# Performance work log

Hardware: AMD Instinct MI355X
Metric: run time of the kernel (lower is better)

## Reference

```python
import jax, jax.numpy as jnp
import numpy as np

N, E, IN_DIM, HID, OUT = 50000, 800000, 256, 128, 128
EPS_BN = 1e-5
EPS_NORM = 1e-12


def leaky(x):
    return jnp.where(x >= 0, x, 0.2 * x)


def batchnorm(x, gamma, beta):
    # training-mode BatchNorm1d over node dimension
    mean = jnp.mean(x, axis=0)
    var = jnp.var(x, axis=0)
    return gamma * (x - mean) * jax.lax.rsqrt(var + EPS_BN) + beta


def sage_conv(x, src, dst, W_l, b_l, W_r):
    # PyG SAGEConv (mean aggr): lin_l(mean_{j->i} x_j) + lin_r(x_i)
    msg = x[src]  # [E, D] gather
    agg = jax.ops.segment_sum(msg, dst, num_segments=N)
    cnt = jax.ops.segment_sum(jnp.ones((E,), x.dtype), dst, num_segments=N)
    agg = agg / jnp.maximum(cnt, 1.0)[:, None]
    return agg @ W_l + b_l + x @ W_r


def setup_inputs() -> dict:
    key = jax.random.key(0)
    ks = jax.random.split(key, 16)
    s = lambda fan_in: (2.0 / fan_in) ** 0.5
    return {
        "x": jax.random.normal(ks[0], (N, IN_DIM), jnp.float32),
        "edge_index": jax.random.randint(ks[1], (2, E), 0, N),
        "W_in": jax.random.normal(ks[2], (IN_DIM, HID), jnp.float32) * s(IN_DIM),
        "b_in": jnp.zeros((HID,), jnp.float32),
        "g1": jnp.ones((HID,), jnp.float32),
        "be1": jnp.zeros((HID,), jnp.float32),
        "Wl1": jax.random.normal(ks[3], (HID, HID), jnp.float32) * s(HID),
        "bl1": jnp.zeros((HID,), jnp.float32),
        "Wr1": jax.random.normal(ks[4], (HID, HID), jnp.float32) * s(HID),
        "Wl2": jax.random.normal(ks[5], (HID, OUT), jnp.float32) * s(HID),
        "bl2": jnp.zeros((OUT,), jnp.float32),
        "Wr2": jax.random.normal(ks[6], (HID, OUT), jnp.float32) * s(HID),
        "Wskip": jax.random.normal(ks[7], (HID, OUT), jnp.float32) * s(HID),
        "bskip": jnp.zeros((OUT,), jnp.float32),
        "g2": jnp.ones((OUT,), jnp.float32),
        "be2": jnp.zeros((OUT,), jnp.float32),
    }


def reference(x, edge_index, W_in, b_in, g1, be1, Wl1, bl1, Wr1, Wl2, bl2, Wr2, Wskip, bskip, g2, be2):
    src, dst = edge_index[0], edge_index[1]
    h = batchnorm(leaky(x @ W_in + b_in), g1, be1)
    skip = h
    h1 = leaky(sage_conv(h, src, dst, Wl1, bl1, Wr1))  # dropout = identity (eval)
    h2 = sage_conv(h1, src, dst, Wl2, bl2, Wr2)
    out = h2 + (skip @ Wskip + bskip)
    out = batchnorm(out, g2, be2)
    norm = jnp.sqrt(jnp.sum(out * out, axis=1, keepdims=True))
    return out / jnp.maximum(norm, EPS_NORM)
```

## Files before the change

kernel.cpp:

```cpp
#include <hip/hip_runtime.h>
#include <math.h>

#define N_NODES 50000
#define N_EDGES 800000
#define IN_DIM 256
#define HID 128
#define ZPITCH 384

typedef unsigned short u16;
typedef u16 u16x8 __attribute__((ext_vector_type(8)));
typedef u16 u16x2 __attribute__((ext_vector_type(2)));
typedef __bf16 bf16x8 __attribute__((ext_vector_type(8)));
typedef float f32x4 __attribute__((ext_vector_type(4)));

#define AS1 __attribute__((address_space(1)))
#define AS3 __attribute__((address_space(3)))

union F8 { u16x8 u; bf16x8 h; };

__device__ __forceinline__ u16 f2b(float f) {
    unsigned u = __builtin_bit_cast(unsigned, f);
    u = (u + 0x7FFFu + ((u >> 16) & 1u)) >> 16;
    return (u16)u;
}
__device__ __forceinline__ float b2f(u16 h) {
    unsigned u = ((unsigned)h) << 16;
    return __builtin_bit_cast(float, u);
}

template<int A_F32> struct ARaw;
template<> struct ARaw<0> { u16x8 v; };
template<> struct ARaw<1> { float4 f0, f1; };

template<int A_F32>
__device__ __forceinline__ ARaw<A_F32> load_raw(const void* base, size_t row, int P, int koff);
template<>
__device__ __forceinline__ ARaw<0> load_raw<0>(const void* base, size_t row, int P, int koff) {
    ARaw<0> r;
    r.v = *reinterpret_cast<const u16x8*>((const u16*)base + row * P + koff);
    return r;
}
template<>
__device__ __forceinline__ ARaw<1> load_raw<1>(const void* base, size_t row, int P, int koff) {
    ARaw<1> r;
    const float* p = (const float*)base + row * P + koff;
    r.f0 = *reinterpret_cast<const float4*>(p);
    r.f1 = *reinterpret_cast<const float4*>(p + 4);
    return r;
}

template<int A_F32>
__device__ __forceinline__ F8 to_frag(const ARaw<A_F32>& r);
template<>
__device__ __forceinline__ F8 to_frag<0>(const ARaw<0>& r) { F8 f; f.u = r.v; return f; }
template<>
__device__ __forceinline__ F8 to_frag<1>(const ARaw<1>& r) {
    F8 f;
    f.h[0] = (__bf16)r.f0.x; f.h[1] = (__bf16)r.f0.y;
    f.h[2] = (__bf16)r.f0.z; f.h[3] = (__bf16)r.f0.w;
    f.h[4] = (__bf16)r.f1.x; f.h[5] = (__bf16)r.f1.y;
    f.h[6] = (__bf16)r.f1.z; f.h[7] = (__bf16)r.f1.w;
    return f;
}

template<int LEAKY, int STATS, int OUT_BF16, int A_F32, int NC>
__global__ __launch_bounds__(512, 2) void gemm_mfma(
    int M, const void* __restrict__ A, int P,
    const u16* __restrict__ Wf,
    const float* __restrict__ bias0,
    void* __restrict__ Cout, int CP,
    float* __restrict__ stats)
{
    __shared__ u16 Bs[NC * 4096];

    const int t   = threadIdx.x;
    const int w   = t >> 6;
    const int l   = t & 63;
    const int l15 = l & 15;
    const int lg  = l >> 4;
    const int rb  = blockIdx.x * 256 + w * 32;

    int r0 = rb + l15;
    int r1 = r0 + 16;
    size_t r0c = (size_t)(r0 < M ? r0 : M - 1);
    size_t r1c = (size_t)(r1 < M ? r1 : M - 1);
    const int ko = lg * 8;

#pragma unroll
    for (int i = 0; i < NC; ++i) {
        int idx = i * 512 + t;
        __builtin_amdgcn_global_load_lds(
            (const AS1 void*)(Wf + (size_t)idx * 8),
            (AS3 void*)(Bs + (size_t)idx * 8), 16, 0, 0);
    }

    constexpr int D = (NC < 4) ? NC : 4;
    ARaw<A_F32> a0[NC], a1[NC];
#pragma unroll
    for (int c = 0; c < D; ++c) {
        a0[c] = load_raw<A_F32>(A, r0c, P, c * 32 + ko);
        a1[c] = load_raw<A_F32>(A, r1c, P, c * 32 + ko);
    }

    __syncthreads();

    f32x4 acc[2][8];
#pragma unroll
    for (int m = 0; m < 2; ++m)
#pragma unroll
        for (int j = 0; j < 8; ++j) acc[m][j] = 0.0f;

    F8 b[8], nb[8];
#pragma unroll
    for (int j = 0; j < 8; ++j)
        b[j].u = *reinterpret_cast<const u16x8*>(Bs + (size_t)(j * 64 + l) * 8);

#pragma unroll
    for (int c = 0; c < NC; ++c) {
        if (c + D < NC) {
            a0[c + D] = load_raw<A_F32>(A, r0c, P, (c + D) * 32 + ko);
            a1[c + D] = load_raw<A_F32>(A, r1c, P, (c + D) * 32 + ko);
        }
        if (c + 1 < NC) {
#pragma unroll
            for (int j = 0; j < 8; ++j)
                nb[j].u = *reinterpret_cast<const u16x8*>(
                    Bs + (size_t)(((c + 1) * 8 + j) * 64 + l) * 8);
        }
        F8 fa0 = to_frag<A_F32>(a0[c]);
        F8 fa1 = to_frag<A_F32>(a1[c]);
#pragma unroll
        for (int j = 0; j < 8; ++j) {
            acc[0][j] = __builtin_amdgcn_mfma_f32_16x16x32_bf16(fa0.h, b[j].h, acc[0][j], 0, 0, 0);
            acc[1][j] = __builtin_amdgcn_mfma_f32_16x16x32_bf16(fa1.h, b[j].h, acc[1][j], 0, 0, 0);
        }
#pragma unroll
        for (int j = 0; j < 8; ++j) b[j] = nb[j];
    }

    float bias_j[8];
#pragma unroll
    for (int j = 0; j < 8; ++j) bias_j[j] = bias0[16 * j + l15];

    float csum[8], csq[8];
#pragma unroll
    for (int j = 0; j < 8; ++j) { csum[j] = 0.f; csq[j] = 0.f; }

#pragma unroll
    for (int m = 0; m < 2; ++m) {
        int rbase = rb + m * 16 + lg * 4;
#pragma unroll
        for (int r = 0; r < 4; ++r) {
            int row = rbase + r;
            bool ok = row < M;
#pragma unroll
            for (int j = 0; j < 8; ++j) {
                float y = acc[m][j][r] + bias_j[j];
                if (LEAKY) y = (y >= 0.f) ? y : 0.2f * y;
                if (ok) {
                    if (OUT_BF16)
                        ((u16*)Cout)[(size_t)row * CP + 16 * j + l15] = f2b(y);
                    else
                        ((float*)Cout)[(size_t)row * CP + 16 * j + l15] = y;
                    if (STATS) { csum[j] += y; csq[j] += y * y; }
                }
            }
        }
    }

    if (STATS) {
        __shared__ float sred[256];
        if (t < 256) sred[t] = 0.f;
        __syncthreads();
#pragma unroll
        for (int j = 0; j < 8; ++j) {
            float s = csum[j];
            float q = csq[j];
            s += __shfl_xor(s, 16); s += __shfl_xor(s, 32);
            q += __shfl_xor(q, 16); q += __shfl_xor(q, 32);
            if (lg == 0) {
                atomicAdd(&sred[16 * j + l15], s);
                atomicAdd(&sred[128 + 16 * j + l15], q);
            }
        }
        __syncthreads();
        if (t < 256) atomicAdd(&stats[t], sred[t]);
    }
}

__global__ __launch_bounds__(256) void conv_w(const float* s0, const float* s1, const float* s2,
                                              const float* sc0, const float* sc1, const float* sc2,
                                              int rows_each, u16* __restrict__ dst, int nchunks)
{
    int tid = blockIdx.x * 256 + threadIdx.x;
    if (tid >= nchunks * 512) return;
    int c   = tid >> 9;
    int j   = (tid >> 6) & 7;
    int l   = tid & 63;
    int l15 = l & 15, lg = l >> 4;

    int srow0 = c * 32;
    int si    = srow0 / rows_each;
    const float* S  = (si == 0) ? s0 : (si == 1) ? s1 : s2;
    const float* SC = (si == 0) ? sc0 : (si == 1) ? sc1 : sc2;
    int rbase = srow0 - si * rows_each + lg * 8;
    int col   = 16 * j + l15;

    u16x8 o;
#pragma unroll
    for (int i = 0; i < 8; ++i) {
        float v = S[(size_t)(rbase + i) * HID + col];
        if (SC) v *= SC[rbase + i];
        o[i] = f2b(v);
    }
    reinterpret_cast<u16x8*>(dst)[tid] = o;
}

__global__ void bias_fold(const float* __restrict__ b0, const float* __restrict__ b1,
                          const float* __restrict__ W0, const float* __restrict__ W1,
                          const float* __restrict__ sh, float* __restrict__ outb)
{
    int j = threadIdx.x;
    float acc = b0[j] + (b1 ? b1[j] : 0.f);
    for (int i = 0; i < HID; ++i) {
        float w = W0[(size_t)i * HID + j] + (W1 ? W1[(size_t)i * HID + j] : 0.f);
        acc = fmaf(sh[i], w, acc);
    }
    outb[j] = acc;
}

__global__ void bn_params(const float* __restrict__ stats,
                          const float* __restrict__ gamma,
                          const float* __restrict__ beta,
                          float* __restrict__ scale,
                          float* __restrict__ shift, float invn)
{
    int j = threadIdx.x;
    float mean = stats[j] * invn;
    float var  = stats[128 + j] * invn - mean * mean;
    var = fmaxf(var, 0.f);
    float sc = gamma[j] / sqrtf(var + 1e-5f);
    scale[j] = sc;
    shift[j] = beta[j] - mean * sc;
}

__global__ __launch_bounds__(256) void edge_count(const int* __restrict__ dst, int* __restrict__ cnt)
{
    int e = blockIdx.x * 256 + threadIdx.x;
    if (e < N_EDGES) atomicAdd(&cnt[dst[e]], 1);
}

__global__ __launch_bounds__(256) void scan_block(const int* __restrict__ cnt,
                                                  int* __restrict__ excl,
                                                  int* __restrict__ bsum, int n)
{
    __shared__ int sh[256];
    int t = threadIdx.x;
    int i = blockIdx.x * 256 + t;
    int v = (i < n) ? cnt[i] : 0;
    sh[t] = v;
    __syncthreads();
#pragma unroll
    for (int off = 1; off < 256; off <<= 1) {
        int x = (t >= off) ? sh[t - off] : 0;
        __syncthreads();
        sh[t] += x;
        __syncthreads();
    }
    if (i < n) excl[i] = sh[t] - v;
    if (t == 255) bsum[blockIdx.x] = sh[255];
}

__global__ __launch_bounds__(256) void scan_bsum(int* __restrict__ bsum, int nb)
{
    __shared__ int sh[256];
    int t = threadIdx.x;
    int v = (t < nb) ? bsum[t] : 0;
    sh[t] = v;
    __syncthreads();
#pragma unroll
    for (int off = 1; off < 256; off <<= 1) {
        int x = (t >= off) ? sh[t - off] : 0;
        __syncthreads();
        sh[t] += x;
        __syncthreads();
    }
    if (t < nb) bsum[t] = sh[t] - v;
}

__global__ __launch_bounds__(256) void scan_add(int* __restrict__ row_ptr,
                                                int* __restrict__ fillrp,
                                                const int* __restrict__ bsum, int n)
{
    int i = blockIdx.x * 256 + threadIdx.x;
    if (i < n) {
        int v = row_ptr[i] + bsum[i >> 8];
        row_ptr[i] = v;
        fillrp[i]  = v;
    }
    if (i == 0) row_ptr[n] = N_EDGES;
}

#define FILL_EPB 4096
__global__ __launch_bounds__(256) void edge_fill_part(const int* __restrict__ src,
                                                      const int* __restrict__ dst,
                                                      int* __restrict__ fillrp,
                                                      int* __restrict__ col_idx)
{
    const int range = blockIdx.x & 7;
    const int base  = (blockIdx.x >> 3) * FILL_EPB;
    const int lo = range * 6250, hi = lo + 6250;
#pragma unroll
    for (int k = 0; k < FILL_EPB / 256; ++k) {
        int e = base + k * 256 + threadIdx.x;
        if (e < N_EDGES) {
            int d = dst[e];
            if (d >= lo && d < hi) {
                int pos = atomicAdd(&fillrp[d], 1);
                col_idx[pos] = src[e];
            }
        }
    }
}

__global__ __launch_bounds__(256) void spmm_mean(const int* __restrict__ row_ptr,
                                                 const int* __restrict__ col_idx,
                                                 const u16* __restrict__ Z_in,
                                                 u16* __restrict__ Z_out)
{
    int node = blockIdx.x * 4 + (threadIdx.x >> 6);
    if (node >= N_NODES) return;
    int lane = threadIdx.x & 63;
    int beg = row_ptr[node];
    int end = row_ptr[node + 1];

    float sx = 0.f, sy = 0.f;
    int e = beg;
    for (; e + 4 <= end; e += 4) {
        int c0 = col_idx[e], c1 = col_idx[e + 1], c2 = col_idx[e + 2], c3 = col_idx[e + 3];
        u16x2 v0 = *reinterpret_cast<const u16x2*>(Z_in + (size_t)c0 * ZPITCH + lane * 2);
        u16x2 v1 = *reinterpret_cast<const u16x2*>(Z_in + (size_t)c1 * ZPITCH + lane * 2);
        u16x2 v2 = *reinterpret_cast<const u16x2*>(Z_in + (size_t)c2 * ZPITCH + lane * 2);
        u16x2 v3 = *reinterpret_cast<const u16x2*>(Z_in + (size_t)c3 * ZPITCH + lane * 2);
        sx += (b2f(v0[0]) + b2f(v1[0])) + (b2f(v2[0]) + b2f(v3[0]));
        sy += (b2f(v0[1]) + b2f(v1[1])) + (b2f(v2[1]) + b2f(v3[1]));
    }
    for (; e < end; ++e) {
        int c = col_idx[e];
        u16x2 v = *reinterpret_cast<const u16x2*>(Z_in + (size_t)c * ZPITCH + lane * 2);
        sx += b2f(v[0]); sy += b2f(v[1]);
    }
    float inv = 1.f / fmaxf((float)(end - beg), 1.f);
    u16x2 r; r[0] = f2b(sx * inv); r[1] = f2b(sy * inv);
    *reinterpret_cast<u16x2*>(Z_out + (size_t)node * ZPITCH + lane * 2) = r;
}

__global__ __launch_bounds__(256) void bn_rownorm(float* __restrict__ out,
                                                  const float* __restrict__ scale,
                                                  const float* __restrict__ shift)
{
    int row = blockIdx.x * 4 + (threadIdx.x >> 6);
    if (row >= N_NODES) return;
    int lane = threadIdx.x & 63;
    float2 v  = *reinterpret_cast<const float2*>(&out[(size_t)row * HID + lane * 2]);
    float2 sc = *reinterpret_cast<const float2*>(&scale[lane * 2]);
    float2 sh = *reinterpret_cast<const float2*>(&shift[lane * 2]);
    float y0 = v.x * sc.x + sh.x;
    float y1 = v.y * sc.y + sh.y;
    float ss = y0 * y0 + y1 * y1;
#pragma unroll
    for (int m = 1; m < 64; m <<= 1) ss += __shfl_xor(ss, m);
    float inv = 1.f / fmaxf(sqrtf(ss), 1e-12f);
    float2 r = {y0 * inv, y1 * inv};
    *reinterpret_cast<float2*>(&out[(size_t)row * HID + lane * 2]) = r;
}

extern "C" void kernel_launch(void* const* d_in, const int* in_sizes, int n_in,
                              void* d_out, int out_size, void* d_ws, size_t ws_size,
                              hipStream_t stream)
{
    const float* x     = (const float*)d_in[0];
    const int*   ei    = (const int*)d_in[1];
    const float* W_in  = (const float*)d_in[2];
    const float* b_in  = (const float*)d_in[3];
    const float* g1    = (const float*)d_in[4];
    const float* be1   = (const float*)d_in[5];
    const float* Wl1   = (const float*)d_in[6];
    const float* bl1   = (const float*)d_in[7];
    const float* Wr1   = (const float*)d_in[8];
    const float* Wl2   = (const float*)d_in[9];
    const float* bl2   = (const float*)d_in[10];
    const float* Wr2   = (const float*)d_in[11];
    const float* Wskip = (const float*)d_in[12];
    const float* bskip = (const float*)d_in[13];
    const float* g2    = (const float*)d_in[14];
    const float* be2   = (const float*)d_in[15];
    float* out = (float*)d_out;

    char* ws = (char*)d_ws;
    u16*  Z  = (u16*)ws;
    char* zzone = ws + 38400000;
    float* stats = (float*)zzone;
    int*   icnt  = (int*)(zzone + 2048);
    size_t zsz   = 2048 + (size_t)N_NODES * 4;
    int*   row_ptr = (int*)(zzone + zsz);
    int*   fillrp  = (int*)(zzone + zsz + 200064);
    int*   bsum    = (int*)(zzone + zsz + 400128);
    int*   col_idx = (int*)(zzone + zsz + 400128 + 1024);
    float* bnc     = (float*)(zzone + zsz + 400128 + 1024 + (size_t)N_EDGES * 4);
    u16* WfA = (u16*)((char*)bnc + 4096);
    u16* WfB = WfA + 8 * 4096;
    u16* WfC = WfB + 8 * 4096;

    hipMemsetAsync(zzone, 0, zsz, stream);

    const int* srcp = ei;
    const int* dstp = ei + N_EDGES;

    float* scale1 = bnc;
    float* shift1 = bnc + 128;
    float* scale2 = bnc + 256;
    float* shift2 = bnc + 384;
    float* b1eff  = bnc + 512;
    float* b2eff  = bnc + 640;

    conv_w<<<16, 256, 0, stream>>>(W_in, nullptr, nullptr, nullptr, nullptr, nullptr,
                                   256, WfA, 8);

    const int NB = (N_NODES + 255) / 256;
    edge_count<<<(N_EDGES + 255) / 256, 256, 0, stream>>>(dstp, icnt);
    scan_block<<<NB, 256, 0, stream>>>(icnt, row_ptr, bsum, N_NODES);
    scan_bsum<<<1, 256, 0, stream>>>(bsum, NB);
    scan_add<<<NB, 256, 0, stream>>>(row_ptr, fillrp, bsum, N_NODES);
    edge_fill_part<<<((N_EDGES + FILL_EPB - 1) / FILL_EPB) * 8, 256, 0, stream>>>(
        srcp, dstp, fillrp, col_idx);

    const int GB = (N_NODES + 255) / 256;

    gemm_mfma<1, 1, 1, 1, 8><<<GB, 512, 0, stream>>>(
        N_NODES, x, IN_DIM, WfA, b_in, Z + 128, ZPITCH, stats);
    bn_params<<<1, 128, 0, stream>>>(stats, g1, be1, scale1, shift1, 1.f / N_NODES);

    conv_w<<<16, 256, 0, stream>>>(Wl1, Wr1, nullptr, scale1, scale1, nullptr,
                                   128, WfB, 8);
    conv_w<<<24, 256, 0, stream>>>(Wl2, Wskip, Wr2, nullptr, scale1, nullptr,
                                   128, WfC, 12);
    bias_fold<<<1, 128, 0, stream>>>(bl1, nullptr, Wl1, Wr1, shift1, b1eff);
    bias_fold<<<1, 128, 0, stream>>>(bl2, bskip, Wskip, nullptr, shift1, b2eff);

    spmm_mean<<<(N_NODES + 3) / 4, 256, 0, stream>>>(row_ptr, col_idx, Z + 128, Z);
    gemm_mfma<1, 0, 1, 0, 8><<<GB, 512, 0, stream>>>(
        N_NODES, Z, ZPITCH, WfB, b1eff, Z + 256, ZPITCH, nullptr);

    spmm_mean<<<(N_NODES + 3) / 4, 256, 0, stream>>>(row_ptr, col_idx, Z + 256, Z);
    gemm_mfma<0, 1, 0, 0, 12><<<GB, 512, 0, stream>>>(
        N_NODES, Z, ZPITCH, WfC, b2eff, out, HID, stats + 256);

    bn_params<<<1, 128, 0, stream>>>(stats + 256, g2, be2, scale2, shift2, 1.f / N_NODES);
    bn_rownorm<<<(N_NODES + 3) / 4, 256, 0, stream>>>(out, scale2, shift2);
}
```

Before: 268.6 us.

## Split interleaved Z buffer into dense arrays and stage GEMM epilogue through LDS

```diff
diff --git a/kernel.cpp b/kernel.cpp
--- a/kernel.cpp
+++ b/kernel.cpp
@@ -5,7 +5,6 @@
 #define N_EDGES 800000
 #define IN_DIM 256
 #define HID 128
-#define ZPITCH 384
 
 typedef unsigned short u16;
 typedef u16 u16x8 __attribute__((ext_vector_type(8)));
@@ -63,15 +62,17 @@
     return f;
 }
 
-template<int LEAKY, int STATS, int OUT_BF16, int A_F32, int NC>
+template<int LEAKY, int STATS, int OUT_BF16, int A_F32, int NC, int C0, int C1>
 __global__ __launch_bounds__(512, 2) void gemm_mfma(
-    int M, const void* __restrict__ A, int P,
+    int M,
+    const void* __restrict__ A0, const void* __restrict__ A1, const void* __restrict__ A2,
     const u16* __restrict__ Wf,
     const float* __restrict__ bias0,
-    void* __restrict__ Cout, int CP,
+    void* __restrict__ Cout,
     float* __restrict__ stats)
 {
     __shared__ u16 Bs[NC * 4096];
+    __shared__ float sred[256];
 
     const int t   = threadIdx.x;
     const int w   = t >> 6;
@@ -94,13 +95,18 @@
             (AS3 void*)(Bs + (size_t)idx * 8), 16, 0, 0);
     }
 
-    constexpr int D = (NC < 4) ? NC : 4;
-    ARaw<A_F32> a0[NC], a1[NC];
-#pragma unroll
-    for (int c = 0; c < D; ++c) {
-        a0[c] = load_raw<A_F32>(A, r0c, P, c * 32 + ko);
-        a1[c] = load_raw<A_F32>(A, r1c, P, c * 32 + ko);
-    }
+    auto loadA = [&](int c, size_t row) -> ARaw<A_F32> {
+        if (A_F32) {
+            return load_raw<A_F32>(A0, row, IN_DIM, c * 32 + ko);
+        } else {
+            const void* S = (c < C0) ? A0 : (c < C1) ? A1 : A2;
+            int base      = (c < C0) ? 0  : (c < C1) ? C0 : C1;
+            return load_raw<A_F32>(S, row, HID, (c - base) * 32 + ko);
+        }
+    };
+
+    ARaw<A_F32> a0c = loadA(0, r0c);
+    ARaw<A_F32> a1c = loadA(0, r1c);
 
     __syncthreads();
 
@@ -115,25 +121,25 @@
     for (int j = 0; j < 8; ++j)
         b[j].u = *reinterpret_cast<const u16x8*>(Bs + (size_t)(j * 64 + l) * 8);
 
+    ARaw<A_F32> a0n, a1n;
 #pragma unroll
     for (int c = 0; c < NC; ++c) {
-        if (c + D < NC) {
-            a0[c + D] = load_raw<A_F32>(A, r0c, P, (c + D) * 32 + ko);
-            a1[c + D] = load_raw<A_F32>(A, r1c, P, (c + D) * 32 + ko);
-        }
         if (c + 1 < NC) {
+            a0n = loadA(c + 1, r0c);
+            a1n = loadA(c + 1, r1c);
 #pragma unroll
             for (int j = 0; j < 8; ++j)
                 nb[j].u = *reinterpret_cast<const u16x8*>(
                     Bs + (size_t)(((c + 1) * 8 + j) * 64 + l) * 8);
         }
-        F8 fa0 = to_frag<A_F32>(a0[c]);
-        F8 fa1 = to_frag<A_F32>(a1[c]);
+        F8 fa0 = to_frag<A_F32>(a0c);
+        F8 fa1 = to_frag<A_F32>(a1c);
 #pragma unroll
         for (int j = 0; j < 8; ++j) {
             acc[0][j] = __builtin_amdgcn_mfma_f32_16x16x32_bf16(fa0.h, b[j].h, acc[0][j], 0, 0, 0);
             acc[1][j] = __builtin_amdgcn_mfma_f32_16x16x32_bf16(fa1.h, b[j].h, acc[1][j], 0, 0, 0);
         }
+        a0c = a0n; a1c = a1n;
 #pragma unroll
         for (int j = 0; j < 8; ++j) b[j] = nb[j];
     }
@@ -146,30 +152,78 @@
 #pragma unroll
     for (int j = 0; j < 8; ++j) { csum[j] = 0.f; csq[j] = 0.f; }
 
-#pragma unroll
-    for (int m = 0; m < 2; ++m) {
-        int rbase = rb + m * 16 + lg * 4;
-#pragma unroll
-        for (int r = 0; r < 4; ++r) {
-            int row = rbase + r;
-            bool ok = row < M;
-#pragma unroll
-            for (int j = 0; j < 8; ++j) {
-                float y = acc[m][j][r] + bias_j[j];
-                if (LEAKY) y = (y >= 0.f) ? y : 0.2f * y;
-                if (ok) {
-                    if (OUT_BF16)
-                        ((u16*)Cout)[(size_t)row * CP + 16 * j + l15] = f2b(y);
-                    else
-                        ((float*)Cout)[(size_t)row * CP + 16 * j + l15] = y;
-                    if (STATS) { csum[j] += y; csq[j] += y * y; }
+    if (OUT_BF16) {
+        __syncthreads();
+        u16* Cs = Bs;
+#pragma unroll
+        for (int m = 0; m < 2; ++m) {
+#pragma unroll
+            for (int r = 0; r < 4; ++r) {
+                int rl = w * 32 + m * 16 + lg * 4 + r;
+                bool ok = (blockIdx.x * 256 + rl) < M;
+                int S = (rl & 7) << 3;
+#pragma unroll
+                for (int j = 0; j < 8; ++j) {
+                    float y = acc[m][j][r] + bias_j[j];
+                    if (LEAKY) y = (y >= 0.f) ? y : 0.2f * y;
+                    Cs[rl * 128 + ((16 * j + l15) ^ S)] = f2b(y);
+                    if (STATS && ok) { csum[j] += y; csq[j] += y * y; }
                 }
             }
         }
+        __syncthreads();
+        int row  = t >> 1;
+        int kb   = (t & 1) * 8;
+        int grow = blockIdx.x * 256 + row;
+        if (grow < M) {
+#pragma unroll
+            for (int i = 0; i < 8; ++i) {
+                int k = kb + i;
+                u16x8 rd = *reinterpret_cast<const u16x8*>(
+                    Cs + row * 128 + ((k ^ (row & 7)) * 8));
+                *reinterpret_cast<u16x8*>((u16*)Cout + (size_t)grow * 128 + k * 8) = rd;
+            }
+        }
+    } else {
+        float* Cs32 = (float*)Bs;
+#pragma unroll
+        for (int p = 0; p < 2; ++p) {
+            __syncthreads();
+            if ((w >> 2) == p) {
+#pragma unroll
+                for (int m = 0; m < 2; ++m) {
+#pragma unroll
+                    for (int r = 0; r < 4; ++r) {
+                        int rl = (w & 3) * 32 + m * 16 + lg * 4 + r;
+                        bool ok = (blockIdx.x * 256 + p * 128 + rl) < M;
+                        int S = (rl & 7) << 2;
+#pragma unroll
+                        for (int j = 0; j < 8; ++j) {
+                            float y = acc[m][j][r] + bias_j[j];
+                            if (LEAKY) y = (y >= 0.f) ? y : 0.2f * y;
+                            Cs32[rl * 128 + ((16 * j + l15) ^ S)] = y;
+                            if (STATS && ok) { csum[j] += y; csq[j] += y * y; }
+                        }
+                    }
+                }
+            }
+            __syncthreads();
+            int rowl = t >> 2;
+            int qb   = (t & 3) * 8;
+            int grow = blockIdx.x * 256 + p * 128 + rowl;
+            if (grow < M) {
+#pragma unroll
+                for (int i = 0; i < 8; ++i) {
+                    int k = qb + i;
+                    f32x4 rd = *reinterpret_cast<const f32x4*>(
+                        Cs32 + rowl * 128 + ((k ^ (rowl & 7)) * 4));
+                    *reinterpret_cast<f32x4*>((float*)Cout + (size_t)grow * 128 + k * 4) = rd;
+                }
+            }
+        }
     }
 
     if (STATS) {
-        __shared__ float sred[256];
         if (t < 256) sred[t] = 0.f;
         __syncthreads();
 #pragma unroll
@@ -325,8 +379,8 @@
 
 __global__ __launch_bounds__(256) void spmm_mean(const int* __restrict__ row_ptr,
                                                  const int* __restrict__ col_idx,
-                                                 const u16* __restrict__ Z_in,
-                                                 u16* __restrict__ Z_out)
+                                                 const u16* __restrict__ Hin,
+                                                 u16* __restrict__ Aout)
 {
     int node = blockIdx.x * 4 + (threadIdx.x >> 6);
     if (node >= N_NODES) return;
@@ -338,21 +392,21 @@
     int e = beg;
     for (; e + 4 <= end; e += 4) {
         int c0 = col_idx[e], c1 = col_idx[e + 1], c2 = col_idx[e + 2], c3 = col_idx[e + 3];
-        u16x2 v0 = *reinterpret_cast<const u16x2*>(Z_in + (size_t)c0 * ZPITCH + lane * 2);
-        u16x2 v1 = *reinterpret_cast<const u16x2*>(Z_in + (size_t)c1 * ZPITCH + lane * 2);
-        u16x2 v2 = *reinterpret_cast<const u16x2*>(Z_in + (size_t)c2 * ZPITCH + lane * 2);
-        u16x2 v3 = *reinterpret_cast<const u16x2*>(Z_in + (size_t)c3 * ZPITCH + lane * 2);
+        u16x2 v0 = *reinterpret_cast<const u16x2*>(Hin + (size_t)c0 * HID + lane * 2);
+        u16x2 v1 = *reinterpret_cast<const u16x2*>(Hin + (size_t)c1 * HID + lane * 2);
+        u16x2 v2 = *reinterpret_cast<const u16x2*>(Hin + (size_t)c2 * HID + lane * 2);
+        u16x2 v3 = *reinterpret_cast<const u16x2*>(Hin + (size_t)c3 * HID + lane * 2);
         sx += (b2f(v0[0]) + b2f(v1[0])) + (b2f(v2[0]) + b2f(v3[0]));
         sy += (b2f(v0[1]) + b2f(v1[1])) + (b2f(v2[1]) + b2f(v3[1]));
     }
     for (; e < end; ++e) {
         int c = col_idx[e];
-        u16x2 v = *reinterpret_cast<const u16x2*>(Z_in + (size_t)c * ZPITCH + lane * 2);
+        u16x2 v = *reinterpret_cast<const u16x2*>(Hin + (size_t)c * HID + lane * 2);
         sx += b2f(v[0]); sy += b2f(v[1]);
     }
     float inv = 1.f / fmaxf((float)(end - beg), 1.f);
     u16x2 r; r[0] = f2b(sx * inv); r[1] = f2b(sy * inv);
-    *reinterpret_cast<u16x2*>(Z_out + (size_t)node * ZPITCH + lane * 2) = r;
+    *reinterpret_cast<u16x2*>(Aout + (size_t)node * HID + lane * 2) = r;
 }
 
 __global__ __launch_bounds__(256) void bn_rownorm(float* __restrict__ out,
@@ -397,9 +451,12 @@
     const float* be2   = (const float*)d_in[15];
     float* out = (float*)d_out;
 
+    const size_t NB16 = (size_t)N_NODES * HID;
     char* ws = (char*)d_ws;
-    u16*  Z  = (u16*)ws;
-    char* zzone = ws + 38400000;
+    u16* AGG = (u16*)ws;
+    u16* H   = AGG + NB16;
+    u16* H1  = H + NB16;
+    char* zzone = ws + 3 * NB16 * 2;
     float* stats = (float*)zzone;
     int*   icnt  = (int*)(zzone + 2048);
     size_t zsz   = 2048 + (size_t)N_NODES * 4;
@@ -437,8 +494,8 @@
 
     const int GB = (N_NODES + 255) / 256;
 
-    gemm_mfma<1, 1, 1, 1, 8><<<GB, 512, 0, stream>>>(
-        N_NODES, x, IN_DIM, WfA, b_in, Z + 128, ZPITCH, stats);
+    gemm_mfma<1, 1, 1, 1, 8, 8, 8><<<GB, 512, 0, stream>>>(
+        N_NODES, x, nullptr, nullptr, WfA, b_in, H, stats);
     bn_params<<<1, 128, 0, stream>>>(stats, g1, be1, scale1, shift1, 1.f / N_NODES);
 
     conv_w<<<16, 256, 0, stream>>>(Wl1, Wr1, nullptr, scale1, scale1, nullptr,
@@ -448,13 +505,13 @@
     bias_fold<<<1, 128, 0, stream>>>(bl1, nullptr, Wl1, Wr1, shift1, b1eff);
     bias_fold<<<1, 128, 0, stream>>>(bl2, bskip, Wskip, nullptr, shift1, b2eff);
 
-    spmm_mean<<<(N_NODES + 3) / 4, 256, 0, stream>>>(row_ptr, col_idx, Z + 128, Z);
-    gemm_mfma<1, 0, 1, 0, 8><<<GB, 512, 0, stream>>>(
-        N_NODES, Z, ZPITCH, WfB, b1eff, Z + 256, ZPITCH, nullptr);
-
-    spmm_mean<<<(N_NODES + 3) / 4, 256, 0, stream>>>(row_ptr, col_idx, Z + 256, Z);
-    gemm_mfma<0, 1, 0, 0, 12><<<GB, 512, 0, stream>>>(
-        N_NODES, Z, ZPITCH, WfC, b2eff, out, HID, stats + 256);
+    spmm_mean<<<(N_NODES + 3) / 4, 256, 0, stream>>>(row_ptr, col_idx, H, AGG);
+    gemm_mfma<1, 0, 1, 0, 8, 4, 8><<<GB, 512, 0, stream>>>(
+        N_NODES, AGG, H, nullptr, WfB, b1eff, H1, nullptr);
+
+    spmm_mean<<<(N_NODES + 3) / 4, 256, 0, stream>>>(row_ptr, col_idx, H1, AGG);
+    gemm_mfma<0, 1, 0, 0, 12, 4, 8><<<GB, 512, 0, stream>>>(
+        N_NODES, AGG, H, H1, WfC, b2eff, out, stats + 256);
 
     bn_params<<<1, 128, 0, stream>>>(stats + 256, g2, be2, scale2, shift2, 1.f / N_NODES);
     bn_rownorm<<<(N_NODES + 3) / 4, 256, 0, stream>>>(out, scale2, shift2);
```

Measured after the change: 278.9 us. 1.04x slower.
